# Kernel tuning notes

Measured on AMD Instinct MI355X. Metric: run time of the kernel, lower is better.

The kernel has to match this reference:

```python
import jax, jax.numpy as jnp
import numpy as np

C = 64
EPS_LN = 1e-5
EPS_BN = 1e-5


def _conv1x1(x, w, b):
    # x: (B,C,H,W), w: (O,I), b: (O,)
    return jnp.einsum('oi,bihw->bohw', w, x) + b[None, :, None, None]


def _cross_attn(x_a, x_b, wq, bq, wk, bk, wv, bv):
    # query from x_a, key/value from x_b; residual onto x_a
    b, c, h, w = x_a.shape
    hw = h * w
    scale = 1.0 / jnp.sqrt(jnp.asarray(C, x_a.dtype))
    q = _conv1x1(x_a, wq, bq).reshape(b, -1, hw)   # (B,C,HW)
    k = _conv1x1(x_b, wk, bk).reshape(b, -1, hw)   # (B,C,HW)
    v = _conv1x1(x_b, wv, bv).reshape(b, -1, hw)   # (B,C,HW)
    # torch: bmm(k^T, q) -> (B,HW,HW), softmax over last dim
    logits = jnp.einsum('bci,bcj->bij', k, q) * scale
    attn = jax.nn.softmax(logits, axis=-1)
    out = jnp.einsum('bci,bij->bcj', v, attn).reshape(b, -1, h, w)
    return out + x_a


def _layernorm_ch(x, g, b):
    # LayerNorm over channel dim of (B,C,H,W)
    mu = jnp.mean(x, axis=1, keepdims=True)
    var = jnp.var(x, axis=1, keepdims=True)
    xn = (x - mu) * jax.lax.rsqrt(var + EPS_LN)
    return xn * g[None, :, None, None] + b[None, :, None, None]


def setup_inputs() -> dict:
    key = jax.random.key(0)
    ks = jax.random.split(key, 20)
    B, H, W = 4, 64, 64
    s = 0.05
    d = {
        'x_s2': jax.random.normal(ks[0], (B, C, H, W), jnp.float32),
        'x_dem': jax.random.normal(ks[1], (B, C, H, W), jnp.float32),
        'wq1': jax.random.normal(ks[2], (C, C), jnp.float32) * s,
        'bq1': jnp.zeros((C,), jnp.float32),
        'wk1': jax.random.normal(ks[3], (C, C), jnp.float32) * s,
        'bk1': jnp.zeros((C,), jnp.float32),
        'wv1': jax.random.normal(ks[4], (C, C), jnp.float32) * s,
        'bv1': jnp.zeros((C,), jnp.float32),
        'wq2': jax.random.normal(ks[5], (C, C), jnp.float32) * s,
        'bq2': jnp.zeros((C,), jnp.float32),
        'wk2': jax.random.normal(ks[6], (C, C), jnp.float32) * s,
        'bk2': jnp.zeros((C,), jnp.float32),
        'wv2': jax.random.normal(ks[7], (C, C), jnp.float32) * s,
        'bv2': jnp.zeros((C,), jnp.float32),
        'ln_s2_w': jnp.ones((C,), jnp.float32),
        'ln_s2_b': jnp.zeros((C,), jnp.float32),
        'ln_dem_w': jnp.ones((C,), jnp.float32),
        'ln_dem_b': jnp.zeros((C,), jnp.float32),
        'fw1': jax.random.normal(ks[8], (C, 2 * C, 3, 3), jnp.float32) * s,
        'fb1': jnp.zeros((C,), jnp.float32),
        'bn_g': jnp.ones((C,), jnp.float32),
        'bn_b': jnp.zeros((C,), jnp.float32),
        'fw2': jax.random.normal(ks[9], (C, C), jnp.float32) * s,
        'fb2': jnp.zeros((C,), jnp.float32),
    }
    return d


def reference(x_s2, x_dem, wq1, bq1, wk1, bk1, wv1, bv1,
              wq2, bq2, wk2, bk2, wv2, bv2,
              ln_s2_w, ln_s2_b, ln_dem_w, ln_dem_b,
              fw1, fb1, bn_g, bn_b, fw2, fb2):
    out_s2 = _cross_attn(x_s2, x_dem, wq1, bq1, wk1, bk1, wv1, bv1)
    out_dem = _cross_attn(x_dem, x_s2, wq2, bq2, wk2, bk2, wv2, bv2)
    out_s2 = _layernorm_ch(out_s2, ln_s2_w, ln_s2_b)
    out_dem = _layernorm_ch(out_dem, ln_dem_w, ln_dem_b)
    combined = jnp.concatenate([out_s2, out_dem], axis=1)  # (B,2C,H,W)
    y = jax.lax.conv_general_dilated(
        combined, fw1, window_strides=(1, 1), padding='SAME',
        dimension_numbers=('NCHW', 'OIHW', 'NCHW')) + fb1[None, :, None, None]
    # BatchNorm2d in training mode: batch statistics over (B,H,W)
    mu = jnp.mean(y, axis=(0, 2, 3), keepdims=True)
    var = jnp.var(y, axis=(0, 2, 3), keepdims=True)
    y = (y - mu) * jax.lax.rsqrt(var + EPS_BN)
    y = y * bn_g[None, :, None, None] + bn_b[None, :, None, None]
    y = jax.nn.relu(y)
    return _conv1x1(y, fw2, fb2)
```

## Files before the change

kernel.cpp:

```cpp
#include <hip/hip_runtime.h>
#include <hip/hip_bf16.h>


using bf16x8 = __attribute__((ext_vector_type(8))) short;
using f32x4  = __attribute__((ext_vector_type(4))) float;
using f32x16 = __attribute__((ext_vector_type(16))) float;
typedef unsigned int uint2v __attribute__((ext_vector_type(2)));

#define MFMA16(a, b, c) __builtin_amdgcn_mfma_f32_16x16x32_bf16((a), (b), (c), 0, 0, 0)
#define MFMA32(a, b, c) __builtin_amdgcn_mfma_f32_32x32x16_bf16((a), (b), (c), 0, 0, 0)

constexpr int B_ = 4, C_ = 64, S_ = 4096;
constexpr float kQS = 0.18033688f;

constexpr size_t OFF_XT   = 0;
constexpr size_t OFF_WB   = 4u * 1024 * 1024;
constexpr size_t OFF_FW1R = OFF_WB + 64 * 1024;
constexpr size_t OFF_QT   = OFF_FW1R + 160 * 1024;
constexpr size_t OFF_KT   = OFF_QT + 4u * 1024 * 1024;
constexpr size_t OFF_V    = OFF_KT + 4u * 1024 * 1024;
constexpr size_t OFF_COMB = OFF_V + 4u * 1024 * 1024;
constexpr size_t OFF_Y    = OFF_COMB + 4u * 1024 * 1024;
constexpr size_t OFF_PART = OFF_Y + 4u * 1024 * 1024;
constexpr size_t OFF_BNA  = OFF_PART + 128 * 1024;
constexpr size_t OFF_BNB  = OFF_BNA + 1024;

__device__ __forceinline__ unsigned short f2bf(float f) {
  unsigned int u = __float_as_uint(f);
  unsigned int r = (u + 0x7fffu + ((u >> 16) & 1u)) >> 16;
  return (unsigned short)r;
}
__device__ __forceinline__ unsigned int cvt_pk_bf16(float lo, float hi) {
  unsigned int r;
  asm("v_cvt_pk_bf16_f32 %0, %1, %2" : "=v"(r) : "v"(lo), "v"(hi));
  return r;
}
__device__ __forceinline__ float fast_exp2(float x) {
#if __has_builtin(__builtin_amdgcn_exp2f)
  return __builtin_amdgcn_exp2f(x);
#else
  return exp2f(x);
#endif
}
__device__ __forceinline__ void plswap(unsigned int& a, unsigned int& b) {
  uint2v r = __builtin_amdgcn_permlane32_swap(a, b, false, false);
  a = r[0];
  b = r[1];
}
__device__ __forceinline__ void gload_lds16(const void* g, char* lds) {
  __builtin_amdgcn_global_load_lds(
      (const __attribute__((address_space(1))) unsigned int*)g,
      (__attribute__((address_space(3))) unsigned int*)lds, 16, 0, 0);
}

__device__ __forceinline__ void build_pv_frags(const f32x16 s, float& lsum,
                                               bf16x8* out) {
  float p[16];
#pragma unroll
  for (int r = 0; r < 16; ++r) p[r] = fast_exp2(s[r]);
  lsum += (((p[0] + p[1]) + (p[2] + p[3])) + ((p[4] + p[5]) + (p[6] + p[7]))) +
          (((p[8] + p[9]) + (p[10] + p[11])) + ((p[12] + p[13]) + (p[14] + p[15])));
#pragma unroll
  for (int h = 0; h < 2; ++h) {
    unsigned int X  = cvt_pk_bf16(p[8 * h + 0], p[8 * h + 1]);
    unsigned int X2 = cvt_pk_bf16(p[8 * h + 2], p[8 * h + 3]);
    unsigned int Y  = cvt_pk_bf16(p[8 * h + 4], p[8 * h + 5]);
    unsigned int Y2 = cvt_pk_bf16(p[8 * h + 6], p[8 * h + 7]);
    plswap(X, Y);
    plswap(X2, Y2);
    union { unsigned int u[4]; bf16x8 v; } bb;
    bb.u[0] = X; bb.u[1] = X2; bb.u[2] = Y; bb.u[3] = Y2;
    out[h] = bb.v;
  }
}

__global__ void k_prep(const float* wq1, const float* wk1, const float* wv1,
                       const float* wq2, const float* wk2, const float* wv2,
                       const float* fw2, const float* fw1,
                       const float* xs2, const float* xdem,
                       unsigned short* wb, unsigned short* fw1r,
                       unsigned short* xT) {
  __shared__ float lds[64][65];
  if (blockIdx.x < 400) {
    int g = blockIdx.x * 256 + threadIdx.x;
    if (g < 7 * 4096) {
      int m = g >> 12, idx = g & 4095;
      const float* src[7] = {wq1, wk1, wv1, wq2, wk2, wv2, fw2};
      float sc = (m == 0 || m == 3) ? kQS : 1.0f;
      wb[g] = f2bf(src[m][idx] * sc);
    } else {
      int t = g - 7 * 4096;
      if (t < 64 * 1152) {
        int o = t / 1152, kk = t % 1152;
        int dydx = kk >> 7, ci = kk & 127;
        fw1r[t] = f2bf(fw1[o * 1152 + ci * 9 + dydx]);
      }
    }
    return;
  }
  int bid = blockIdx.x - 400;
  int pt = bid & 63, b = (bid >> 6) & 3, tz = bid >> 8;
  int tid = threadIdx.x;
  const float* src = (tz == 0) ? xs2 : xdem;
  int p0 = pt * 64;
#pragma unroll
  for (int k = 0; k < 16; ++k) {
    int idx = k * 256 + tid;
    int c = idx >> 6, pp = idx & 63;
    lds[c][pp] = src[((size_t)(b * 64 + c) << 12) + p0 + pp];
  }
  __syncthreads();
  unsigned short* dst = xT + (size_t)tz * (B_ * S_ * C_);
#pragma unroll
  for (int k = 0; k < 4; ++k) {
    int p = (tid >> 4) + k * 16;
    int c0 = (tid & 15) * 4;
    ushort4 v;
    v.x = f2bf(lds[c0 + 0][p]);
    v.y = f2bf(lds[c0 + 1][p]);
    v.z = f2bf(lds[c0 + 2][p]);
    v.w = f2bf(lds[c0 + 3][p]);
    *(ushort4*)&dst[((size_t)((b << 12) + p0 + p)) * 64 + c0] = v;
  }
}

__global__ __launch_bounds__(256) void k_proj(
    const unsigned short* xT, const unsigned short* wb,
    const float* bq1, const float* bk1, const float* bv1,
    const float* bq2, const float* bk2, const float* bv2,
    unsigned short* Qt, unsigned short* Kt, unsigned short* V) {
  int pc = blockIdx.x, b = blockIdx.y, dir = blockIdx.z;
  int lane = threadIdx.x & 63, wid = threadIdx.x >> 6;
  int l4 = lane & 15, g4 = lane >> 4;
  const unsigned short* xq =
      xT + ((size_t)(dir * B_ + b)) * (size_t)(S_ * C_);
  const unsigned short* xkv =
      xT + ((size_t)((1 - dir) * B_ + b)) * (size_t)(S_ * C_);
  size_t dbOff = ((size_t)dir * B_ + b) * (size_t)(S_ * C_);
  const float* bq = dir ? bq2 : bq1;
  const float* bk = dir ? bk2 : bk1;
  const float* bv = dir ? bv2 : bv1;
  int pbase = pc * 64 + wid * 16;

  bf16x8 aq[2], akv[2];
#pragma unroll
  for (int kc = 0; kc < 2; ++kc) {
    aq[kc] = *(const bf16x8*)&xq[(size_t)(pbase + l4) * 64 + kc * 32 + g4 * 8];
    akv[kc] = *(const bf16x8*)&xkv[(size_t)(pbase + l4) * 64 + kc * 32 + g4 * 8];
  }

#pragma unroll
  for (int prod = 0; prod < 2; ++prod) {
    const unsigned short* wm = wb + (dir * 3 + prod) * 4096;
    unsigned short* dst = (prod == 0 ? Qt : Kt) + dbOff;
    const float* bp = (prod == 0) ? bq : bk;
    float bscale = (prod == 0) ? kQS : 1.0f;
    const bf16x8* af = (prod == 0) ? aq : akv;
#pragma unroll
    for (int nt = 0; nt < 4; ++nt) {
      bf16x8 wf0 = *(const bf16x8*)&wm[(nt * 16 + l4) * 64 + g4 * 8];
      bf16x8 wf1 = *(const bf16x8*)&wm[(nt * 16 + l4) * 64 + 32 + g4 * 8];
      f32x4 acc = {0.f, 0.f, 0.f, 0.f};
      acc = MFMA16(af[0], wf0, acc);
      acc = MFMA16(af[1], wf1, acc);
      float bias_c = bp[nt * 16 + l4] * bscale;
#pragma unroll
      for (int r = 0; r < 4; ++r)
        dst[(size_t)(pbase + g4 * 4 + r) * 64 + nt * 16 + l4] = f2bf(acc[r] + bias_c);
    }
  }
  {
    const unsigned short* wm = wb + (dir * 3 + 2) * 4096;
    unsigned short* dst = V + dbOff;
#pragma unroll
    for (int mt = 0; mt < 4; ++mt) {
      bf16x8 wf0 = *(const bf16x8*)&wm[(mt * 16 + l4) * 64 + g4 * 8];
      bf16x8 wf1 = *(const bf16x8*)&wm[(mt * 16 + l4) * 64 + 32 + g4 * 8];
      f32x4 acc = {0.f, 0.f, 0.f, 0.f};
      acc = MFMA16(wf0, akv[0], acc);
      acc = MFMA16(wf1, akv[1], acc);
#pragma unroll
      for (int r = 0; r < 4; ++r) {
        int c = mt * 16 + g4 * 4 + r;
        dst[(size_t)c * S_ + pbase + l4] = f2bf(acc[r] + bv[c]);
      }
    }
  }
}

constexpr int TST = 72;

__global__ __launch_bounds__(512, 4) void k_attn(
    const unsigned short* Qt, const unsigned short* Kt, const unsigned short* V,
    const float* xs2, const float* xdem,
    const float* lnw_s2, const float* lnb_s2,
    const float* lnw_dem, const float* lnb_dem,
    unsigned short* comb) {
  __shared__ __align__(16) char smem[76800];
  const f32x16 kZero16 = {0.f, 0.f, 0.f, 0.f, 0.f, 0.f, 0.f, 0.f,
                          0.f, 0.f, 0.f, 0.f, 0.f, 0.f, 0.f, 0.f};
  int bd = blockIdx.x, jb = blockIdx.y;
  int dir = bd >> 2, b = bd & 3;
  int lane = threadIdx.x & 63, wid = threadIdx.x >> 6;
  int ih = wid >> 1, jw = wid & 1;
  int l5 = lane & 31;
  int h = lane >> 5;
  int hi8 = h * 8, hi4 = h * 4;
  size_t dbOff = (size_t)bd * (size_t)(S_ * C_);
  const unsigned short* qp = Qt + dbOff;
  const unsigned short* kp = Kt + dbOff;
  const unsigned short* vp = V + dbOff;

  int lr3 = lane >> 3, l7 = lane & 7;
  int swz = l7 ^ lr3;
  size_t goff[4];
  const unsigned short* gsrc;
  if (jw == 0) {
    gsrc = kp;
#pragma unroll
    for (int k = 0; k < 4; ++k) goff[k] = (size_t)(k * 8 + lr3) * 64 + swz * 8;
  } else {
    gsrc = vp;
#pragma unroll
    for (int k = 0; k < 4; ++k) {
      int r = k * 8 + lr3;
      int c = r + ((swz & 4) << 3);
      goff[k] = (size_t)c * 4096 + (swz & 3) * 8;
    }
  }
  char* region = smem + ih * 16384;
  int akoff[4], avoff[4];
#pragma unroll
  for (int k = 0; k < 4; ++k) {
    akoff[k] = l5 * 128 + (((2 * k + h) ^ (l5 & 7)) << 4);
    avoff[k] = 4096 + l5 * 128 + (((2 * k + h) ^ (l5 & 7)) << 4);
  }

  int jbase = jb * 64 + jw * 32;
  bf16x8 qf[4];
  {
    const unsigned short* qrow = qp + (size_t)(jbase + l5) * 64 + hi8;
#pragma unroll
    for (int kc = 0; kc < 4; ++kc) qf[kc] = *(const bf16x8*)(qrow + kc * 16);
  }

  f32x16 acc0 = kZero16, acc1 = kZero16;
  float lsum = 0.f;
  int ibeg = ih * 1024;

#define STAGE(I0, BUF)                                                      \
  {                                                                         \
    size_t so_ = (jw == 0) ? (size_t)(I0) * 64 : (size_t)(I0);              \
    char* d_ = region + (BUF) * 8192 + jw * 4096;                           \
    _Pragma("unroll") for (int k_ = 0; k_ < 4; ++k_)                        \
        gload_lds16(gsrc + so_ + goff[k_], d_ + k_ * 1024);                 \
  }

  STAGE(ibeg, 0)
  STAGE(ibeg + 32, 1)
  asm volatile("s_waitcnt vmcnt(0)" ::: "memory");
  __builtin_amdgcn_s_barrier();
  __builtin_amdgcn_sched_barrier(0);

  int cur = 0;
  for (int t = 0; t < 32; ++t) {
    const char* kb = region + cur * 8192;
    bf16x8 ak[4], av[4];
#pragma unroll
    for (int k = 0; k < 4; ++k) ak[k] = *(const bf16x8*)(kb + akoff[k]);
#pragma unroll
    for (int k = 0; k < 4; ++k) av[k] = *(const bf16x8*)(kb + avoff[k]);
    asm volatile("s_waitcnt lgkmcnt(0)" ::: "memory");
    __builtin_amdgcn_sched_barrier(0);
    __builtin_amdgcn_s_barrier();
    __builtin_amdgcn_sched_barrier(0);
    int i2 = ibeg + ((t + 2) & 31) * 32;
    STAGE(i2, cur)

    __builtin_amdgcn_s_setprio(1);
    f32x16 S = kZero16;
    S = MFMA32(ak[0], qf[0], S);
    S = MFMA32(ak[1], qf[1], S);
    S = MFMA32(ak[2], qf[2], S);
    S = MFMA32(ak[3], qf[3], S);
    __builtin_amdgcn_s_setprio(0);
    bf16x8 pb[2];
    build_pv_frags(S, lsum, pb);
    __builtin_amdgcn_s_setprio(1);
    acc0 = MFMA32(av[0], pb[0], acc0);
    acc0 = MFMA32(av[1], pb[1], acc0);
    acc1 = MFMA32(av[2], pb[0], acc1);
    acc1 = MFMA32(av[3], pb[1], acc1);
    __builtin_amdgcn_s_setprio(0);

    asm volatile("s_waitcnt vmcnt(4)" ::: "memory");
    __builtin_amdgcn_sched_barrier(0);
    __builtin_amdgcn_s_barrier();
    __builtin_amdgcn_sched_barrier(0);
    cur ^= 1;
  }
#undef STAGE

  asm volatile("s_waitcnt vmcnt(0)" ::: "memory");
  __syncthreads();

  float* Lp = (float*)(smem + 65536);
  Lp[wid * 64 + lane] = lsum;

#define STORE1(A_, CIDX, RG)                                              \
  {                                                                       \
    _Pragma("unroll") for (int q2 = 0; q2 < 4; ++q2) {                    \
      f32x4 tv = {(A_)[q2 * 4 + 0], (A_)[q2 * 4 + 1],                     \
                  (A_)[q2 * 4 + 2], (A_)[q2 * 4 + 3]};                    \
      *(f32x4*)&(RG)[((CIDX) * 4 + q2) * 256 + lane * 4] = tv;            \
    }                                                                     \
  }
#define ADD1(A_, CIDX, RR)                                                \
  {                                                                       \
    _Pragma("unroll") for (int q2 = 0; q2 < 4; ++q2) {                    \
      f32x4 tv = *(const f32x4*)&(RR)[((CIDX) * 4 + q2) * 256 + lane * 4];\
      _Pragma("unroll") for (int e = 0; e < 4; ++e) (A_)[q2 * 4 + e] += tv[e]; \
    }                                                                     \
  }
#define PUB(SLOT)                                                         \
  {                                                                       \
    float* rg_ = (float*)(smem + (size_t)(SLOT) * 8192);                  \
    STORE1(acc0, 0, rg_) STORE1(acc1, 1, rg_)                             \
  }
#define ADDP(SLOT)                                                        \
  {                                                                       \
    const float* rr_ = (const float*)(smem + (size_t)(SLOT) * 8192);      \
    ADD1(acc0, 0, rr_) ADD1(acc1, 1, rr_)                                 \
  }

  if (ih >= 2) PUB((ih - 2) * 2 + jw)
  __syncthreads();
  if (ih < 2) {
    ADDP(ih * 2 + jw)
    if (ih == 1) PUB(2 + jw)
  }
  __syncthreads();
  if (ih != 0) return;
  ADDP(2 + jw)
#undef PUB
#undef ADDP
#undef STORE1
#undef ADD1

  float ls = 0.f;
#pragma unroll
  for (int ihh = 0; ihh < 4; ++ihh) ls += Lp[(ihh * 2 + jw) * 64 + lane];
  ls += __shfl_xor(ls, 32);
  float linv = 1.0f / ls;

  const float* xa = (dir == 0 ? xs2 : xdem) + (size_t)b * C_ * S_;
  const float* lw = (dir == 0) ? lnw_s2 : lnw_dem;
  const float* lbp = (dir == 0) ? lnb_s2 : lnb_dem;
  int jcol = jbase + l5;

  float vals[32];
  float s1 = 0.f, s2 = 0.f;
#pragma unroll
  for (int ct = 0; ct < 2; ++ct)
#pragma unroll
    for (int reg = 0; reg < 16; ++reg) {
      int c = ct * 32 + (reg & 3) + 8 * (reg >> 2) + hi4;
      float v = (ct ? acc1[reg] : acc0[reg]) * linv + xa[(size_t)c * S_ + jcol];
      vals[ct * 16 + reg] = v;
      s1 += v;
      s2 += v * v;
    }
  s1 += __shfl_xor(s1, 32);
  s2 += __shfl_xor(s2, 32);
  float mean = s1 * (1.0f / 64.0f);
  float var = s2 * (1.0f / 64.0f) - mean * mean;
  float rstd = rsqrtf(var + 1e-5f);

  unsigned short* T = (unsigned short*)(smem + 67584 + jw * 4608);
#pragma unroll
  for (int ct = 0; ct < 2; ++ct)
#pragma unroll
    for (int q2 = 0; q2 < 4; ++q2)
#pragma unroll
      for (int pp = 0; pp < 2; ++pp) {
        int r0 = q2 * 4 + pp * 2;
        int c0 = ct * 32 + 8 * q2 + hi4 + pp * 2;
        float x0 = (vals[ct * 16 + r0 + 0] - mean) * rstd * lw[c0 + 0] + lbp[c0 + 0];
        float x1 = (vals[ct * 16 + r0 + 1] - mean) * rstd * lw[c0 + 1] + lbp[c0 + 1];
        *(unsigned int*)&T[l5 * TST + c0] = cvt_pk_bf16(x0, x1);
      }
  int j_l = lane >> 1, cc = (lane & 1) * 32;
  unsigned short* cb =
      comb + ((size_t)b * S_ + jbase + j_l) * 128 + dir * 64 + cc;
  const unsigned short* ts = &T[j_l * TST + cc];
#pragma unroll
  for (int q = 0; q < 4; ++q) {
    uint4 tq = *(const uint4*)&ts[q * 8];
    *(uint4*)&cb[q * 8] = tq;
  }
}

__global__ __launch_bounds__(256) void k_conv3(const unsigned short* comb,
                                               const unsigned short* fw1r,
                                               const float* fb1, float* y,
                                               float* part) {
  __shared__ float red[4][128];
  int pc = blockIdx.x, b = blockIdx.y;
  int lane = threadIdx.x & 63, wid = threadIdx.x >> 6;
  int l4 = lane & 15, g4 = lane >> 4;
  int p0 = pc * 64 + wid * 16;
  int p_l = p0 + l4;
  int py0 = p_l >> 6, px0 = p_l & 63;
  f32x4 acc[4];
#pragma unroll
  for (int ot = 0; ot < 4; ++ot) acc[ot] = f32x4{0.f, 0.f, 0.f, 0.f};

#pragma unroll
  for (int kk9 = 0; kk9 < 9; ++kk9) {
    int py = py0 + (kk9 / 3) - 1;
    int px = px0 + (kk9 % 3) - 1;
    bool ok = (py >= 0) && (py < 64) && (px >= 0) && (px < 64);
    const unsigned short* base = comb + ((size_t)(b << 12) + py * 64 + px) * 128;
#pragma unroll
    for (int kc = 0; kc < 4; ++kc) {
      bf16x8 af = {0, 0, 0, 0, 0, 0, 0, 0};
      if (ok) af = *(const bf16x8*)&base[kc * 32 + g4 * 8];
#pragma unroll
      for (int ot = 0; ot < 4; ++ot) {
        bf16x8 bfr = *(const bf16x8*)&fw1r[(size_t)(ot * 16 + l4) * 1152 + kk9 * 128 + kc * 32 + g4 * 8];
        acc[ot] = MFMA16(af, bfr, acc[ot]);
      }
    }
  }
  float ps[4], ps2[4];
#pragma unroll
  for (int ot = 0; ot < 4; ++ot) {
    float bias = fb1[ot * 16 + l4];
    float s = 0.f, s2 = 0.f;
#pragma unroll
    for (int r = 0; r < 4; ++r) {
      float v = acc[ot][r] + bias;
      y[((size_t)(b << 12) + p0 + g4 * 4 + r) * 64 + ot * 16 + l4] = v;
      s += v;
      s2 += v * v;
    }
    s += __shfl_xor(s, 16);
    s += __shfl_xor(s, 32);
    s2 += __shfl_xor(s2, 16);
    s2 += __shfl_xor(s2, 32);
    ps[ot] = s;
    ps2[ot] = s2;
  }
  if (lane < 16) {
#pragma unroll
    for (int ot = 0; ot < 4; ++ot) {
      red[wid][ot * 16 + lane] = ps[ot];
      red[wid][64 + ot * 16 + lane] = ps2[ot];
    }
  }
  __syncthreads();
  if (wid == 0) {
    int o = lane;
    float s = red[0][o] + red[1][o] + red[2][o] + red[3][o];
    float s2 = red[0][64 + o] + red[1][64 + o] + red[2][64 + o] + red[3][64 + o];
    int blk = b * 64 + pc;
    part[(blk * 64 + o) * 2 + 0] = s;
    part[(blk * 64 + o) * 2 + 1] = s2;
  }
}

__global__ void k_bnfin(const float* part, const float* bng, const float* bnb,
                        float* bnA, float* bnB) {
  int o = threadIdx.x;
  float s = 0.f, s2 = 0.f;
  for (int k = 0; k < 256; ++k) {
    s += part[(k * 64 + o) * 2 + 0];
    s2 += part[(k * 64 + o) * 2 + 1];
  }
  float mean = s * (1.0f / 16384.0f);
  float var = s2 * (1.0f / 16384.0f) - mean * mean;
  float a = bng[o] * rsqrtf(var + 1e-5f);
  bnA[o] = a;
  bnB[o] = bnb[o] - mean * a;
}

__global__ __launch_bounds__(128) void k_final(const float* y, const unsigned short* fw2b,
                                               const float* bnA, const float* bnB,
                                               const float* fb2, float* out) {
  int pc = blockIdx.x, b = blockIdx.y;
  int lane = threadIdx.x & 63, wid = threadIdx.x >> 6;
  int l4 = lane & 15, g4 = lane >> 4;
  int p0 = pc * 32 + wid * 16;

  bf16x8 afw[4][2];
#pragma unroll
  for (int mt = 0; mt < 4; ++mt)
#pragma unroll
    for (int kc = 0; kc < 2; ++kc)
      afw[mt][kc] = *(const bf16x8*)&fw2b[(mt * 16 + l4) * 64 + kc * 32 + g4 * 8];
  float a8[2][8], b8[2][8];
#pragma unroll
  for (int kc = 0; kc < 2; ++kc)
#pragma unroll
    for (int e = 0; e < 8; ++e) {
      int c = kc * 32 + g4 * 8 + e;
      a8[kc][e] = bnA[c];
      b8[kc][e] = bnB[c];
    }
  float fbv[4][4];
#pragma unroll
  for (int mt = 0; mt < 4; ++mt)
#pragma unroll
    for (int r = 0; r < 4; ++r) fbv[mt][r] = fb2[mt * 16 + g4 * 4 + r];

  f32x4 acc[4];
#pragma unroll
  for (int mt = 0; mt < 4; ++mt) acc[mt] = f32x4{0.f, 0.f, 0.f, 0.f};

#pragma unroll
  for (int kc = 0; kc < 2; ++kc) {
    const float* yrow = &y[((size_t)(b << 12) + p0 + l4) * 64 + kc * 32 + g4 * 8];
    float4 y0 = *(const float4*)yrow;
    float4 y1 = *(const float4*)(yrow + 4);
    float zv[8] = {y0.x, y0.y, y0.z, y0.w, y1.x, y1.y, y1.z, y1.w};
    bf16x8 zf;
#pragma unroll
    for (int e = 0; e < 8; ++e)
      zf[e] = (short)f2bf(fmaxf(zv[e] * a8[kc][e] + b8[kc][e], 0.f));
#pragma unroll
    for (int mt = 0; mt < 4; ++mt) acc[mt] = MFMA16(afw[mt][kc], zf, acc[mt]);
  }
#pragma unroll
  for (int mt = 0; mt < 4; ++mt)
#pragma unroll
    for (int r = 0; r < 4; ++r)
      out[((size_t)b * 64 + mt * 16 + g4 * 4 + r) * (size_t)S_ + p0 + l4] =
          acc[mt][r] + fbv[mt][r];
}

extern "C" void kernel_launch(void* const* d_in, const int* in_sizes, int n_in,
                              void* d_out, int out_size, void* d_ws, size_t ws_size,
                              hipStream_t stream) {
  const float* x_s2 = (const float*)d_in[0];
  const float* x_dem = (const float*)d_in[1];
  const float* wq1 = (const float*)d_in[2];
  const float* bq1 = (const float*)d_in[3];
  const float* wk1 = (const float*)d_in[4];
  const float* bk1 = (const float*)d_in[5];
  const float* wv1 = (const float*)d_in[6];
  const float* bv1 = (const float*)d_in[7];
  const float* wq2 = (const float*)d_in[8];
  const float* bq2 = (const float*)d_in[9];
  const float* wk2 = (const float*)d_in[10];
  const float* bk2 = (const float*)d_in[11];
  const float* wv2 = (const float*)d_in[12];
  const float* bv2 = (const float*)d_in[13];
  const float* ln_s2_w = (const float*)d_in[14];
  const float* ln_s2_b = (const float*)d_in[15];
  const float* ln_dem_w = (const float*)d_in[16];
  const float* ln_dem_b = (const float*)d_in[17];
  const float* fw1 = (const float*)d_in[18];
  const float* fb1 = (const float*)d_in[19];
  const float* bn_g = (const float*)d_in[20];
  const float* bn_b = (const float*)d_in[21];
  const float* fw2 = (const float*)d_in[22];
  const float* fb2 = (const float*)d_in[23];

  char* ws = (char*)d_ws;
  unsigned short* xT = (unsigned short*)(ws + OFF_XT);
  unsigned short* wbuf = (unsigned short*)(ws + OFF_WB);
  unsigned short* fw1r = (unsigned short*)(ws + OFF_FW1R);
  unsigned short* Qt = (unsigned short*)(ws + OFF_QT);
  unsigned short* Kt = (unsigned short*)(ws + OFF_KT);
  unsigned short* V = (unsigned short*)(ws + OFF_V);
  unsigned short* comb = (unsigned short*)(ws + OFF_COMB);
  float* ybuf = (float*)(ws + OFF_Y);
  float* part = (float*)(ws + OFF_PART);
  float* bnA = (float*)(ws + OFF_BNA);
  float* bnB = (float*)(ws + OFF_BNB);

  k_prep<<<912, 256, 0, stream>>>(wq1, wk1, wv1, wq2, wk2, wv2, fw2, fw1,
                                  x_s2, x_dem, wbuf, fw1r, xT);
  k_proj<<<dim3(64, 4, 2), 256, 0, stream>>>(xT, wbuf, bq1, bk1, bv1,
                                             bq2, bk2, bv2, Qt, Kt, V);
  k_attn<<<dim3(8, 64), 512, 0, stream>>>(Qt, Kt, V, x_s2, x_dem,
                                          ln_s2_w, ln_s2_b, ln_dem_w, ln_dem_b,
                                          comb);
  k_conv3<<<dim3(64, 4), 256, 0, stream>>>(comb, fw1r, fb1, ybuf, part);
  k_bnfin<<<1, 64, 0, stream>>>(part, bn_g, bn_b, bnA, bnB);
  k_final<<<dim3(128, 4), 128, 0, stream>>>(ybuf, wbuf + 6 * 4096, bnA, bnB, fb2,
                                            (float*)d_out);
}
```

Baseline: 107.4 us.

## Store Q/K/V in fragment-major layout and load attention operands directly from global

The projection kernel now writes Q, K and V in a 16-element chunked layout that matches the MFMA fragment order. The attention kernel drops its LDS double-buffered staging (global_load_lds, barriers, setprio) and has each wave read K/V fragments straight from global memory. Blocks shrink to 4 waves, each handling 32 queries over a quarter of the keys, so twice as many blocks launch with far less shared memory. This removes per-iteration barriers and LDS traffic but relies on L2/L1 to serve K/V reuse across waves, and loses explicit prefetch overlap.

```diff
diff --git a/kernel.cpp b/kernel.cpp
--- a/kernel.cpp
+++ b/kernel.cpp
@@ -46,11 +46,6 @@
   uint2v r = __builtin_amdgcn_permlane32_swap(a, b, false, false);
   a = r[0];
   b = r[1];
-}
-__device__ __forceinline__ void gload_lds16(const void* g, char* lds) {
-  __builtin_amdgcn_global_load_lds(
-      (const __attribute__((address_space(1))) unsigned int*)g,
-      (__attribute__((address_space(3))) unsigned int*)lds, 16, 0, 0);
 }
 
 __device__ __forceinline__ void build_pv_frags(const f32x16 s, float& lsum,
@@ -128,7 +123,7 @@
     const unsigned short* xT, const unsigned short* wb,
     const float* bq1, const float* bk1, const float* bv1,
     const float* bq2, const float* bk2, const float* bv2,
-    unsigned short* Qt, unsigned short* Kt, unsigned short* V) {
+    unsigned short* Qf, unsigned short* Kf, unsigned short* Vf) {
   int pc = blockIdx.x, b = blockIdx.y, dir = blockIdx.z;
   int lane = threadIdx.x & 63, wid = threadIdx.x >> 6;
   int l4 = lane & 15, g4 = lane >> 4;
@@ -152,7 +147,7 @@
 #pragma unroll
   for (int prod = 0; prod < 2; ++prod) {
     const unsigned short* wm = wb + (dir * 3 + prod) * 4096;
-    unsigned short* dst = (prod == 0 ? Qt : Kt) + dbOff;
+    unsigned short* dst = (prod == 0 ? Qf : Kf) + dbOff;
     const float* bp = (prod == 0) ? bq : bk;
     float bscale = (prod == 0) ? kQS : 1.0f;
     const bf16x8* af = (prod == 0) ? aq : akv;
@@ -166,12 +161,13 @@
       float bias_c = bp[nt * 16 + l4] * bscale;
 #pragma unroll
       for (int r = 0; r < 4; ++r)
-        dst[(size_t)(pbase + g4 * 4 + r) * 64 + nt * 16 + l4] = f2bf(acc[r] + bias_c);
+        dst[(size_t)nt * 65536 + (size_t)(pbase + g4 * 4 + r) * 16 + l4] =
+            f2bf(acc[r] + bias_c);
     }
   }
   {
     const unsigned short* wm = wb + (dir * 3 + 2) * 4096;
-    unsigned short* dst = V + dbOff;
+    unsigned short* dst = Vf + dbOff;
 #pragma unroll
     for (int mt = 0; mt < 4; ++mt) {
       bf16x8 wf0 = *(const bf16x8*)&wm[(mt * 16 + l4) * 64 + g4 * 8];
@@ -182,7 +178,7 @@
 #pragma unroll
       for (int r = 0; r < 4; ++r) {
         int c = mt * 16 + g4 * 4 + r;
-        dst[(size_t)c * S_ + pbase + l4] = f2bf(acc[r] + bv[c]);
+        dst[(size_t)(pbase >> 4) * 1024 + c * 16 + l4] = f2bf(acc[r] + bv[c]);
       }
     }
   }
@@ -190,121 +186,62 @@
 
 constexpr int TST = 72;
 
-__global__ __launch_bounds__(512, 4) void k_attn(
-    const unsigned short* Qt, const unsigned short* Kt, const unsigned short* V,
+__global__ __launch_bounds__(256, 4) void k_attn(
+    const unsigned short* Qf, const unsigned short* Kf, const unsigned short* Vf,
     const float* xs2, const float* xdem,
     const float* lnw_s2, const float* lnb_s2,
     const float* lnw_dem, const float* lnb_dem,
     unsigned short* comb) {
-  __shared__ __align__(16) char smem[76800];
+  __shared__ __align__(16) char smem[17408];
   const f32x16 kZero16 = {0.f, 0.f, 0.f, 0.f, 0.f, 0.f, 0.f, 0.f,
                           0.f, 0.f, 0.f, 0.f, 0.f, 0.f, 0.f, 0.f};
   int bd = blockIdx.x, jb = blockIdx.y;
   int dir = bd >> 2, b = bd & 3;
   int lane = threadIdx.x & 63, wid = threadIdx.x >> 6;
-  int ih = wid >> 1, jw = wid & 1;
   int l5 = lane & 31;
   int h = lane >> 5;
   int hi8 = h * 8, hi4 = h * 4;
   size_t dbOff = (size_t)bd * (size_t)(S_ * C_);
-  const unsigned short* qp = Qt + dbOff;
-  const unsigned short* kp = Kt + dbOff;
-  const unsigned short* vp = V + dbOff;
-
-  int lr3 = lane >> 3, l7 = lane & 7;
-  int swz = l7 ^ lr3;
-  size_t goff[4];
-  const unsigned short* gsrc;
-  if (jw == 0) {
-    gsrc = kp;
-#pragma unroll
-    for (int k = 0; k < 4; ++k) goff[k] = (size_t)(k * 8 + lr3) * 64 + swz * 8;
-  } else {
-    gsrc = vp;
-#pragma unroll
-    for (int k = 0; k < 4; ++k) {
-      int r = k * 8 + lr3;
-      int c = r + ((swz & 4) << 3);
-      goff[k] = (size_t)c * 4096 + (swz & 3) * 8;
-    }
-  }
-  char* region = smem + ih * 16384;
-  int akoff[4], avoff[4];
-#pragma unroll
-  for (int k = 0; k < 4; ++k) {
-    akoff[k] = l5 * 128 + (((2 * k + h) ^ (l5 & 7)) << 4);
-    avoff[k] = 4096 + l5 * 128 + (((2 * k + h) ^ (l5 & 7)) << 4);
-  }
-
-  int jbase = jb * 64 + jw * 32;
+  const unsigned short* qp = Qf + dbOff;
+  const unsigned short* kp = Kf + dbOff;
+  const unsigned short* vp = Vf + dbOff;
+
+  int jbase = jb * 32;
   bf16x8 qf[4];
-  {
-    const unsigned short* qrow = qp + (size_t)(jbase + l5) * 64 + hi8;
-#pragma unroll
-    for (int kc = 0; kc < 4; ++kc) qf[kc] = *(const bf16x8*)(qrow + kc * 16);
-  }
+#pragma unroll
+  for (int kc = 0; kc < 4; ++kc)
+    qf[kc] = *(const bf16x8*)&qp[(size_t)kc * 65536 + (size_t)(jbase + l5) * 16 + hi8];
 
   f32x16 acc0 = kZero16, acc1 = kZero16;
   float lsum = 0.f;
-  int ibeg = ih * 1024;
-
-#define STAGE(I0, BUF)                                                      \
-  {                                                                         \
-    size_t so_ = (jw == 0) ? (size_t)(I0) * 64 : (size_t)(I0);              \
-    char* d_ = region + (BUF) * 8192 + jw * 4096;                           \
-    _Pragma("unroll") for (int k_ = 0; k_ < 4; ++k_)                        \
-        gload_lds16(gsrc + so_ + goff[k_], d_ + k_ * 1024);                 \
-  }
-
-  STAGE(ibeg, 0)
-  STAGE(ibeg + 32, 1)
-  asm volatile("s_waitcnt vmcnt(0)" ::: "memory");
-  __builtin_amdgcn_s_barrier();
-  __builtin_amdgcn_sched_barrier(0);
-
-  int cur = 0;
+  int ibeg = wid * 1024;
+
   for (int t = 0; t < 32; ++t) {
-    const char* kb = region + cur * 8192;
+    int i0 = ibeg + t * 32;
     bf16x8 ak[4], av[4];
 #pragma unroll
-    for (int k = 0; k < 4; ++k) ak[k] = *(const bf16x8*)(kb + akoff[k]);
-#pragma unroll
-    for (int k = 0; k < 4; ++k) av[k] = *(const bf16x8*)(kb + avoff[k]);
-    asm volatile("s_waitcnt lgkmcnt(0)" ::: "memory");
-    __builtin_amdgcn_sched_barrier(0);
-    __builtin_amdgcn_s_barrier();
-    __builtin_amdgcn_sched_barrier(0);
-    int i2 = ibeg + ((t + 2) & 31) * 32;
-    STAGE(i2, cur)
-
-    __builtin_amdgcn_s_setprio(1);
+    for (int k = 0; k < 4; ++k)
+      ak[k] = *(const bf16x8*)&kp[(size_t)k * 65536 + (size_t)(i0 + l5) * 16 + hi8];
+    int ic = i0 >> 4;
+    av[0] = *(const bf16x8*)&vp[(size_t)ic * 1024 + l5 * 16 + hi8];
+    av[1] = *(const bf16x8*)&vp[(size_t)(ic + 1) * 1024 + l5 * 16 + hi8];
+    av[2] = *(const bf16x8*)&vp[(size_t)ic * 1024 + (32 + l5) * 16 + hi8];
+    av[3] = *(const bf16x8*)&vp[(size_t)(ic + 1) * 1024 + (32 + l5) * 16 + hi8];
+
     f32x16 S = kZero16;
     S = MFMA32(ak[0], qf[0], S);
     S = MFMA32(ak[1], qf[1], S);
     S = MFMA32(ak[2], qf[2], S);
     S = MFMA32(ak[3], qf[3], S);
-    __builtin_amdgcn_s_setprio(0);
     bf16x8 pb[2];
     build_pv_frags(S, lsum, pb);
-    __builtin_amdgcn_s_setprio(1);
     acc0 = MFMA32(av[0], pb[0], acc0);
     acc0 = MFMA32(av[1], pb[1], acc0);
     acc1 = MFMA32(av[2], pb[0], acc1);
     acc1 = MFMA32(av[3], pb[1], acc1);
-    __builtin_amdgcn_s_setprio(0);
-
-    asm volatile("s_waitcnt vmcnt(4)" ::: "memory");
-    __builtin_amdgcn_sched_barrier(0);
-    __builtin_amdgcn_s_barrier();
-    __builtin_amdgcn_sched_barrier(0);
-    cur ^= 1;
-  }
-#undef STAGE
-
-  asm volatile("s_waitcnt vmcnt(0)" ::: "memory");
-  __syncthreads();
-
-  float* Lp = (float*)(smem + 65536);
+  }
+
+  float* Lp = (float*)(smem + 16384);
   Lp[wid * 64 + lane] = lsum;
 
 #define STORE1(A_, CIDX, RG)                                              \
@@ -333,15 +270,17 @@
     ADD1(acc0, 0, rr_) ADD1(acc1, 1, rr_)                                 \
   }
 
-  if (ih >= 2) PUB((ih - 2) * 2 + jw)
+  if (wid >= 2) PUB(wid - 2)
   __syncthreads();
-  if (ih < 2) {
-    ADDP(ih * 2 + jw)
-    if (ih == 1) PUB(2 + jw)
+  if (wid == 1) {
+    ADDP(1)
+    PUB(1)
+  } else if (wid == 0) {
+    ADDP(0)
   }
   __syncthreads();
-  if (ih != 0) return;
-  ADDP(2 + jw)
+  if (wid != 0) return;
+  ADDP(1)
 #undef PUB
 #undef ADDP
 #undef STORE1
@@ -349,7 +288,7 @@
 
   float ls = 0.f;
 #pragma unroll
-  for (int ihh = 0; ihh < 4; ++ihh) ls += Lp[(ihh * 2 + jw) * 64 + lane];
+  for (int ihh = 0; ihh < 4; ++ihh) ls += Lp[ihh * 64 + lane];
   ls += __shfl_xor(ls, 32);
   float linv = 1.0f / ls;
 
@@ -376,7 +315,7 @@
   float var = s2 * (1.0f / 64.0f) - mean * mean;
   float rstd = rsqrtf(var + 1e-5f);
 
-  unsigned short* T = (unsigned short*)(smem + 67584 + jw * 4608);
+  unsigned short* T = (unsigned short*)smem;
 #pragma unroll
   for (int ct = 0; ct < 2; ++ct)
 #pragma unroll
@@ -570,9 +509,9 @@
   unsigned short* xT = (unsigned short*)(ws + OFF_XT);
   unsigned short* wbuf = (unsigned short*)(ws + OFF_WB);
   unsigned short* fw1r = (unsigned short*)(ws + OFF_FW1R);
-  unsigned short* Qt = (unsigned short*)(ws + OFF_QT);
-  unsigned short* Kt = (unsigned short*)(ws + OFF_KT);
-  unsigned short* V = (unsigned short*)(ws + OFF_V);
+  unsigned short* Qf = (unsigned short*)(ws + OFF_QT);
+  unsigned short* Kf = (unsigned short*)(ws + OFF_KT);
+  unsigned short* Vf = (unsigned short*)(ws + OFF_V);
   unsigned short* comb = (unsigned short*)(ws + OFF_COMB);
   float* ybuf = (float*)(ws + OFF_Y);
   float* part = (float*)(ws + OFF_PART);
@@ -582,10 +521,10 @@
   k_prep<<<912, 256, 0, stream>>>(wq1, wk1, wv1, wq2, wk2, wv2, fw2, fw1,
                                   x_s2, x_dem, wbuf, fw1r, xT);
   k_proj<<<dim3(64, 4, 2), 256, 0, stream>>>(xT, wbuf, bq1, bk1, bv1,
-                                             bq2, bk2, bv2, Qt, Kt, V);
-  k_attn<<<dim3(8, 64), 512, 0, stream>>>(Qt, Kt, V, x_s2, x_dem,
-                                          ln_s2_w, ln_s2_b, ln_dem_w, ln_dem_b,
-                                          comb);
+                                             bq2, bk2, bv2, Qf, Kf, Vf);
+  k_attn<<<dim3(8, 128), 256, 0, stream>>>(Qf, Kf, Vf, x_s2, x_dem,
+                                           ln_s2_w, ln_s2_b, ln_dem_w, ln_dem_b,
+                                           comb);
   k_conv3<<<dim3(64, 4), 256, 0, stream>>>(comb, fw1r, fb1, ybuf, part);
   k_bnfin<<<1, 64, 0, stream>>>(part, bn_g, bn_b, bnA, bnB);
   k_final<<<dim3(128, 4), 128, 0, stream>>>(ybuf, wbuf + 6 * 4096, bnA, bnB, fb2,
```

New measurement: 101.6 us. -5.4%, faster.
